# Kernel tuning notes

Measured on AMD Instinct MI355X. Metric: run time of the kernel, lower is better.

The kernel has to match this reference:

```python
import jax, jax.numpy as jnp
import numpy as np

B, L, T = 64, 256, 800
NMEL, PRE, ARNN, DRNN, ENC, ATT, NF, K = 80, 256, 512, 512, 512, 128, 32, 31
ZP = 0.1  # zoneout prob (eval-mode expected-value interpolation)


def setup_inputs() -> dict:
    key = jax.random.key(0)
    ks = iter(jax.random.split(key, 32))
    def p(shape, s=0.05):
        return jax.random.normal(next(ks), shape, dtype=jnp.float32) * s
    inp = {
        'encoder_out': jax.random.normal(next(ks), (B, L, ENC), dtype=jnp.float32),
        'lengths': jax.random.randint(next(ks), (B,), L // 2, L + 1),
        'mels': jax.random.normal(next(ks), (B, T, NMEL), dtype=jnp.float32),
        # prenet: 3 bias-free linears with relu (eval: dropout off)
        'Wp1': p((PRE, NMEL)), 'Wp2': p((PRE, PRE)), 'Wp3': p((PRE, PRE)),
        # attention LSTMCell: input = prenet_dim + enc = 768
        'aWih': p((4 * ARNN, PRE + ENC)), 'aWhh': p((4 * ARNN, ARNN)),
        'abih': jnp.zeros((4 * ARNN,)), 'abhh': jnp.zeros((4 * ARNN,)),
        # decoder LSTMCell: input = att_rnn + enc = 1024
        'dWih': p((4 * DRNN, ARNN + ENC)), 'dWhh': p((4 * DRNN, DRNN)),
        'dbih': jnp.zeros((4 * DRNN,)), 'dbhh': jnp.zeros((4 * DRNN,)),
        # location-sensitive attention (all bias-free)
        'Wq': p((ATT, ARNN)), 'Wm': p((ATT, ENC)),
        'Wconv': p((NF, 2, K)), 'Wloc': p((ATT, NF)), 'v': p((1, ATT)),
        # output projection + gate
        'Wout': p((NMEL, DRNN + ENC)), 'bout': jnp.zeros((NMEL,)),
        'Wgate': p((1, DRNN + ENC)), 'bgate': jnp.zeros((1,)),
    }
    return inp


def _lstm(x, h, c, Wih, Whh, bih, bhh):
    g = x @ Wih.T + h @ Whh.T + (bih + bhh)
    i, f, gg, o = jnp.split(g, 4, axis=-1)
    c2 = jax.nn.sigmoid(f) * c + jax.nn.sigmoid(i) * jnp.tanh(gg)
    return jax.nn.sigmoid(o) * jnp.tanh(c2), c2


def _zoneout(new, old):
    return ZP * old + (1.0 - ZP) * new


def decoder_forward(encoder_out, lengths, mels, Wp1, Wp2, Wp3,
                    aWih, aWhh, abih, abhh, dWih, dWhh, dbih, dbhh,
                    Wq, Wm, Wconv, Wloc, v, Wout, bout, Wgate, bgate):
    b, l, _ = encoder_out.shape
    t = mels.shape[1]
    processed_memory = encoder_out @ Wm.T                       # (B,L,ATT)
    mask = jnp.arange(l)[None, :] >= lengths[:, None]           # True = padded
    # teacher forcing inputs: shift mels right by one zero frame
    dec_in = jnp.concatenate(
        [jnp.zeros((b, 1, NMEL), encoder_out.dtype), mels[:, :t - 1]], axis=1)
    xs = jnp.swapaxes(dec_in, 0, 1)                             # (T,B,NMEL)

    def step(carry, frame):
        ah, ac, dh, dc, ctx, aw, aws = carry
        x = jax.nn.relu(jax.nn.relu(jax.nn.relu(frame @ Wp1.T) @ Wp2.T) @ Wp3.T)
        ah2, ac2 = _lstm(jnp.concatenate([x, ctx], -1), ah, ac, aWih, aWhh, abih, abhh)
        ah2, ac2 = _zoneout(ah2, ah), _zoneout(ac2, ac)
        # location features: conv over (B,2,L)
        aw_cat = jnp.stack([aw, aws], axis=1)
        loc = jax.lax.conv_general_dilated(
            aw_cat, Wconv, window_strides=(1,), padding=[((K - 1) // 2,) * 2],
            dimension_numbers=('NCH', 'OIH', 'NCH'))                # (B,NF,L)
        ploc = jnp.swapaxes(loc, 1, 2) @ Wloc.T                      # (B,L,ATT)
        e = jnp.tanh(ah2[:, None, :] @ Wq.T + processed_memory + ploc)
        energies = jnp.squeeze(e @ v.T, -1)                          # (B,L)
        energies = jnp.where(mask, jnp.float32(-1e9), energies)
        w = jax.nn.softmax(energies, axis=-1)
        ctx2 = jnp.einsum('bl,ble->be', w, encoder_out)
        aws2 = aws + w
        dh2, dc2 = _lstm(jnp.concatenate([ah2, ctx2], -1), dh, dc, dWih, dWhh, dbih, dbhh)
        dh2, dc2 = _zoneout(dh2, dh), _zoneout(dc2, dc)
        dhc = jnp.concatenate([dh2, ctx2], axis=-1)
        mel = dhc @ Wout.T + bout
        gate = jnp.squeeze(dhc @ Wgate.T + bgate, -1)
        return (ah2, ac2, dh2, dc2, ctx2, w, aws2), (mel, gate, w)

    z = lambda *s: jnp.zeros(s, encoder_out.dtype)
    carry0 = (z(b, ARNN), z(b, ARNN), z(b, DRNN), z(b, DRNN), z(b, ENC), z(b, l), z(b, l))
    _, (mel_t, gate_t, align_t) = jax.lax.scan(step, carry0, xs)
    return (jnp.swapaxes(mel_t, 0, 1),      # (B,T,NMEL)
            jnp.swapaxes(gate_t, 0, 1),     # (B,T)
            jnp.swapaxes(align_t, 0, 1))    # (B,T,L)


def reference(encoder_out, lengths, mels, Wp1, Wp2, Wp3,
              aWih, aWhh, abih, abhh, dWih, dWhh, dbih, dbhh,
              Wq, Wm, Wconv, Wloc, v, Wout, bout, Wgate, bgate):
    return decoder_forward(encoder_out, lengths, mels, Wp1, Wp2, Wp3,
                           aWih, aWhh, abih, abhh, dWih, dWhh, dbih, dbhh,
                           Wq, Wm, Wconv, Wloc, v, Wout, bout, Wgate, bgate)
```

## Files before the change

kernel.cpp:

```cpp
#include <hip/hip_runtime.h>


#define DEV_INLINE __device__ __forceinline__

constexpr int TB = 800;

constexpr size_t PMT_O = 0;
constexpr size_t GDT_O = 2097152;
constexpr size_t ENG_O = 2228224;
constexpr size_t WQT_O = 2244608;
constexpr size_t AH_O  = 2310144;
constexpr size_t AC_O  = 2375680;
constexpr size_t DH_O  = 2441216;
constexpr size_t DC_O  = 2506752;
constexpr size_t CTX_O = 2572288;
constexpr size_t AW_O  = 2637824;
constexpr size_t AWS_O = 2670592;
constexpr size_t XB_O  = 2703360;

constexpr size_t MEL_O  = 0;
constexpr size_t GATE_O = 4096000;
constexpr size_t ALG_O  = 4147200;

DEV_INLINE float sigf(float x)     { return 1.0f / (1.0f + __expf(-x)); }
DEV_INLINE float tanhfast(float x) { float e = __expf(2.0f * x); return 1.0f - 2.0f / (e + 1.0f); }

template<int NO>
DEV_INLINE void gseg(float* __restrict__ acc,
                     const float* __restrict__ inT,
                     const float* __restrict__ W, const int ldw, const int wcol0,
                     const int* __restrict__ rows, const int segk0, const int seglen,
                     const int ks, const int ke, const int lane)
{
  const int a0 = ks > segk0 ? ks : segk0;
  const int a1 = (ke < segk0 + seglen) ? ke : (segk0 + seglen);
  if (a0 >= a1) return;
  const float* __restrict__ ip = inT + (size_t)(a0 - segk0) * 64 + lane;
  const int n = a1 - a0;
  const float* wp[NO];
#pragma unroll
  for (int j = 0; j < NO; ++j)
    wp[j] = W + (size_t)rows[j] * ldw + (wcol0 + (a0 - segk0));
  for (int k = 0; k < n; k += 4) {
    const float x0 = ip[(k + 0) * 64];
    const float x1 = ip[(k + 1) * 64];
    const float x2 = ip[(k + 2) * 64];
    const float x3 = ip[(k + 3) * 64];
#pragma unroll
    for (int j = 0; j < NO; ++j)
      acc[j] += x0 * wp[j][k] + x1 * wp[j][k + 1] + x2 * wp[j][k + 2] + x3 * wp[j][k + 3];
  }
}

__global__ __launch_bounds__(256) void init_kernel(const float* __restrict__ Wq,
                                                   float* __restrict__ ws)
{
  const int i = blockIdx.x * 256 + threadIdx.x;
  {
    const int k = i >> 7, a = i & 127;
    ws[WQT_O + i] = Wq[a * 512 + k];
  }
  for (size_t idx = i; idx < 393216; idx += 65536)
    ws[AH_O + idx] = 0.0f;
}

__global__ __launch_bounds__(256) void prenet_kernel(const float* __restrict__ mels,
                                                     const float* __restrict__ Wp1,
                                                     const float* __restrict__ Wp2,
                                                     const float* __restrict__ Wp3,
                                                     float* __restrict__ xb, int t0)
{
  __shared__ float smem[16384];
  const int t = t0 + blockIdx.x;
  const int tid = threadIdx.x;
  const int lane = tid & 63;
  const int wv = __builtin_amdgcn_readfirstlane(tid >> 6);

  if (t == 0) {
    for (int i = tid; i < 5200; i += 256) smem[i] = 0.0f;
  } else {
    for (int i = tid; i < 5120; i += 256) {
      const int b = i / 80, k = i - b * 80;
      smem[k * 65 + b] = mels[((size_t)b * TB + (t - 1)) * 80 + k];
    }
  }
  __syncthreads();

  float va[8][8];
#pragma unroll
  for (int g = 0; g < 8; ++g) {
    const int u0 = wv * 64 + g * 8;
    float acc[8] = {};
    for (int k = 0; k < 80; ++k) {
      const float x = smem[k * 65 + lane];
#pragma unroll
      for (int j = 0; j < 8; ++j) acc[j] += x * Wp1[(u0 + j) * 80 + k];
    }
#pragma unroll
    for (int j = 0; j < 8; ++j) va[g][j] = fmaxf(acc[j], 0.0f);
  }
  __syncthreads();
#pragma unroll
  for (int g = 0; g < 8; ++g)
#pragma unroll
    for (int j = 0; j < 8; ++j) smem[(wv * 64 + g * 8 + j) * 64 + lane] = va[g][j];
  __syncthreads();

#pragma unroll
  for (int g = 0; g < 8; ++g) {
    const int u0 = wv * 64 + g * 8;
    float acc[8] = {};
    for (int k = 0; k < 256; ++k) {
      const float x = smem[k * 64 + lane];
#pragma unroll
      for (int j = 0; j < 8; ++j) acc[j] += x * Wp2[(u0 + j) * 256 + k];
    }
#pragma unroll
    for (int j = 0; j < 8; ++j) va[g][j] = fmaxf(acc[j], 0.0f);
  }
  __syncthreads();
#pragma unroll
  for (int g = 0; g < 8; ++g)
#pragma unroll
    for (int j = 0; j < 8; ++j) smem[(wv * 64 + g * 8 + j) * 64 + lane] = va[g][j];
  __syncthreads();

#pragma unroll
  for (int g = 0; g < 8; ++g) {
    const int u0 = wv * 64 + g * 8;
    float acc[8] = {};
    for (int k = 0; k < 256; ++k) {
      const float x = smem[k * 64 + lane];
#pragma unroll
      for (int j = 0; j < 8; ++j) acc[j] += x * Wp3[(u0 + j) * 256 + k];
    }
#pragma unroll
    for (int j = 0; j < 8; ++j)
      xb[((size_t)blockIdx.x * 256 + (u0 + j)) * 64 + lane] = fmaxf(acc[j], 0.0f);
  }
}

__global__ __launch_bounds__(256) void pm_kernel(const float* __restrict__ enc,
                                                 const float* __restrict__ Wm,
                                                 float* __restrict__ pmT)
{
  __shared__ float encL[64 * 129];
  const int b = blockIdx.x >> 2;
  const int l0 = (blockIdx.x & 3) * 64;
  const int tid = threadIdx.x;
  const int lane = tid & 63;
  const int wv = __builtin_amdgcn_readfirstlane(tid >> 6);

  float acc[4][8];
#pragma unroll
  for (int ai = 0; ai < 4; ++ai)
#pragma unroll
    for (int j = 0; j < 8; ++j) acc[ai][j] = 0.0f;

  for (int kc = 0; kc < 4; ++kc) {
    __syncthreads();
    for (int i = tid; i < 64 * 128; i += 256) {
      const int l = i >> 7, k = i & 127;
      encL[l * 129 + k] = enc[((size_t)b * 256 + l0 + l) * 512 + kc * 128 + k];
    }
    __syncthreads();
#pragma unroll
    for (int ai = 0; ai < 4; ++ai) {
      const int agrp = (ai * 4 + wv) * 8;
      for (int k = 0; k < 128; ++k) {
        const float x = encL[lane * 129 + k];
#pragma unroll
        for (int j = 0; j < 8; ++j)
          acc[ai][j] += x * Wm[(size_t)(agrp + j) * 512 + kc * 128 + k];
      }
    }
  }
#pragma unroll
  for (int ai = 0; ai < 4; ++ai) {
    const int agrp = (ai * 4 + wv) * 8;
#pragma unroll
    for (int j = 0; j < 8; ++j)
      pmT[((size_t)b * 128 + agrp + j) * 256 + l0 + lane] = acc[ai][j];
  }
}

__global__ __launch_bounds__(256) void k_alstm(
    const float* __restrict__ xt,  const float* __restrict__ ctx_i,
    const float* __restrict__ ah_i, const float* __restrict__ ac_i,
    float* __restrict__ ah_o, float* __restrict__ ac_o,
    const float* __restrict__ dh_i,
    const float* __restrict__ aWih, const float* __restrict__ aWhh,
    const float* __restrict__ abih, const float* __restrict__ abhh,
    const float* __restrict__ Wout, const float* __restrict__ bout,
    const float* __restrict__ Wgate, const float* __restrict__ bgate,
    float* __restrict__ out, int t, int do_a, int do_m)
{
  __shared__ float sm[2048];
  const int tid = threadIdx.x;
  const int blk = blockIdx.x;
  const int lane = tid & 63;
  const int wv = __builtin_amdgcn_readfirstlane(tid >> 6);

  if (blk < 256) {
    if (!do_a) return;
    const int u0 = blk * 2;
    int rows[8];
#pragma unroll
    for (int j = 0; j < 8; ++j) rows[j] = u0 + (j >> 2) + 512 * (j & 3);
    float acc[8] = {};
    const int ks = wv * 320, ke = ks + 320;
    gseg<8>(acc, xt,    aWih, 768, 0,   rows, 0,   256, ks, ke, lane);
    gseg<8>(acc, ctx_i, aWih, 768, 256, rows, 256, 512, ks, ke, lane);
    gseg<8>(acc, ah_i,  aWhh, 512, 0,   rows, 768, 512, ks, ke, lane);
#pragma unroll
    for (int j = 0; j < 8; ++j) sm[(wv * 8 + j) * 64 + lane] = acc[j];
    __syncthreads();
    if (tid < 128) {
      const int m = tid & 63, uq = tid >> 6;
      const int u = u0 + uq;
      float g[4];
#pragma unroll
      for (int q = 0; q < 4; ++q) {
        const int j = uq * 4 + q;
        const int row = u + 512 * q;
        g[q] = sm[j * 64 + m] + sm[(8 + j) * 64 + m] + sm[(16 + j) * 64 + m] + sm[(24 + j) * 64 + m]
             + abih[row] + abhh[row];
      }
      const float co = ac_i[u * 64 + m], ho = ah_i[u * 64 + m];
      const float c2 = sigf(g[1]) * co + sigf(g[0]) * tanhfast(g[2]);
      const float h2 = sigf(g[3]) * tanhfast(c2);
      ah_o[u * 64 + m] = 0.1f * ho + 0.9f * h2;
      ac_o[u * 64 + m] = 0.1f * co + 0.9f * c2;
    }
  } else if (do_m && blk < 277) {
    if (blk < 276) {
      const int c0 = (blk - 256) * 4;
      int rows[4] = {c0, c0 + 1, c0 + 2, c0 + 3};
      float acc[4] = {};
      const int ks = wv * 256, ke = ks + 256;
      gseg<4>(acc, dh_i,  Wout, 1024, 0,   rows, 0,   512, ks, ke, lane);
      gseg<4>(acc, ctx_i, Wout, 1024, 512, rows, 512, 512, ks, ke, lane);
#pragma unroll
      for (int j = 0; j < 4; ++j) sm[(wv * 4 + j) * 64 + lane] = acc[j];
      __syncthreads();
      {
        const int m = tid & 63, c = tid >> 6;
        const float val = sm[c * 64 + m] + sm[(4 + c) * 64 + m] + sm[(8 + c) * 64 + m] + sm[(12 + c) * 64 + m]
                        + bout[c0 + c];
        out[MEL_O + ((size_t)m * TB + (t - 1)) * 80 + c0 + c] = val;
      }
    } else {
      float acc[1] = {};
      int rows1[1] = {0};
      const int ks = wv * 256, ke = ks + 256;
      gseg<1>(acc, dh_i,  Wgate, 1024, 0,   rows1, 0,   512, ks, ke, lane);
      gseg<1>(acc, ctx_i, Wgate, 1024, 512, rows1, 512, 512, ks, ke, lane);
      sm[wv * 64 + lane] = acc[0];
      __syncthreads();
      if (tid < 64) {
        const float val = sm[tid] + sm[64 + tid] + sm[128 + tid] + sm[192 + tid] + bgate[0];
        out[GATE_O + (size_t)tid * TB + (t - 1)] = val;
      }
    }
  }
}

__global__ __launch_bounds__(256) void k_energy(
    const float* __restrict__ ah2,  const float* __restrict__ dh_i,
    const float* __restrict__ aw_i, const float* __restrict__ aws_i,
    const float* __restrict__ pmT,  const float* __restrict__ wqT,
    float* __restrict__ gdT, float* __restrict__ eng,
    const float* __restrict__ dWih, const float* __restrict__ dWhh,
    const float* __restrict__ dbih, const float* __restrict__ dbhh,
    const float* __restrict__ Wconv, const float* __restrict__ Wloc,
    const float* __restrict__ v, const int* __restrict__ len)
{
  __shared__ float sm[3584];
  const int tid = threadIdx.x;
  const int blk = blockIdx.x;
  const int lane = tid & 63;
  const int wv = __builtin_amdgcn_readfirstlane(tid >> 6);

  if (blk < 256) {
    const int u0 = blk * 2;
    int rows[8];
#pragma unroll
    for (int j = 0; j < 8; ++j) rows[j] = u0 + (j >> 2) + 512 * (j & 3);
    float acc[8] = {};
    const int ks = wv * 256, ke = ks + 256;
    gseg<8>(acc, ah2,  dWih, 1024, 0, rows, 0,   512, ks, ke, lane);
    gseg<8>(acc, dh_i, dWhh, 512,  0, rows, 512, 512, ks, ke, lane);
#pragma unroll
    for (int j = 0; j < 8; ++j) sm[(wv * 8 + j) * 64 + lane] = acc[j];
    __syncthreads();
    if (tid < 128) {
      const int m = tid & 63, uq = tid >> 6;
      const int u = u0 + uq;
#pragma unroll
      for (int q = 0; q < 4; ++q) {
        const int j = uq * 4 + q;
        const int row = u + 512 * q;
        gdT[(size_t)row * 64 + m] =
            sm[j * 64 + m] + sm[(8 + j) * 64 + m] + sm[(16 + j) * 64 + m] + sm[(24 + j) * 64 + m]
          + dbih[row] + dbhh[row];
      }
    }
  } else {
    const int eb = blk - 256;
    const int b = eb >> 2;
    const int l0 = (eb & 3) * 64;
    float* qL   = sm;
    float* a2L  = sm + 128;
    float* awL  = sm + 640;
    float* awsL = sm + 928;
    float* locL = sm + 1216;
    float* pr   = sm + 3328;

    for (int k = tid; k < 512; k += 256) a2L[k] = ah2[(size_t)k * 64 + b];
    if (tid < 15) { awL[tid] = 0.0f; awsL[tid] = 0.0f; awL[271 + tid] = 0.0f; awsL[271 + tid] = 0.0f; }
    awL[15 + tid]  = aw_i[b * 256 + tid];
    awsL[15 + tid] = aws_i[b * 256 + tid];
    __syncthreads();
    {
      const int a = tid & 127, h = tid >> 7;
      float qp = 0.0f;
      const float* wq = wqT + (size_t)(h * 256) * 128 + a;
      const float* xv = a2L + h * 256;
      for (int k = 0; k < 256; k += 4)
        qp += wq[(k + 0) * 128] * xv[k + 0] + wq[(k + 1) * 128] * xv[k + 1]
            + wq[(k + 2) * 128] * xv[k + 2] + wq[(k + 3) * 128] * xv[k + 3];
      locL[h * 128 + a] = qp;
    }
    __syncthreads();
    if (tid < 128) qL[tid] = locL[tid] + locL[128 + tid];
    __syncthreads();
    {
      float awv[31], awsv[31];
#pragma unroll
      for (int k = 0; k < 31; ++k) { awv[k] = awL[l0 + lane + k]; awsv[k] = awsL[l0 + lane + k]; }
      const int f0 = wv * 8;
      for (int f = f0; f < f0 + 8; ++f) {
        const float* wc = Wconv + f * 62;
        float lf = 0.0f;
#pragma unroll
        for (int k = 0; k < 31; ++k) lf += awv[k] * wc[k] + awsv[k] * wc[31 + k];
        locL[lane * 33 + f] = lf;
      }
    }
    __syncthreads();
    {
      float locv[32];
#pragma unroll
      for (int f = 0; f < 32; ++f) locv[f] = locL[lane * 33 + f];
      float part = 0.0f;
      const int a0 = wv * 32;
      const float* pmp = pmT + (size_t)b * 128 * 256 + l0 + lane;
      for (int a = a0; a < a0 + 32; ++a) {
        float s = qL[a] + pmp[(size_t)a * 256];
        const float* wl = Wloc + a * 32;
#pragma unroll
        for (int f = 0; f < 32; ++f) s += locv[f] * wl[f];
        part += v[a] * tanhfast(s);
      }
      pr[wv * 64 + lane] = part;
    }
    __syncthreads();
    if (tid < 64) {
      float e = pr[tid] + pr[64 + tid] + pr[128 + tid] + pr[192 + tid];
      const int l = l0 + tid;
      if (l >= len[b]) e = -1e9f;
      eng[b * 256 + l] = e;
    }
  }
}

__global__ __launch_bounds__(256) void k_ctx(
    const float* __restrict__ eng, const float* __restrict__ enc,
    const float* __restrict__ aws_i,
    float* __restrict__ ctx_o, float* __restrict__ aw_o, float* __restrict__ aws_o,
    float* __restrict__ out, int t)
{
  __shared__ float sm[896];
  const int tid = threadIdx.x;
  const int lane = tid & 63;
  const int wv = __builtin_amdgcn_readfirstlane(tid >> 6);
  const int b = blockIdx.x >> 2;
  const int ec = blockIdx.x & 3;
  const int e0 = ec * 128;
  float* eL = sm;
  float* wL = sm + 256;
  float* red = sm + 512;
  float* partL = sm + 640;

  eL[tid] = eng[b * 256 + tid];
  __syncthreads();
  float vv = eL[tid];
  for (int mm = 32; mm >= 1; mm >>= 1) vv = fmaxf(vv, __shfl_xor(vv, mm, 64));
  if (lane == 0) red[wv] = vv;
  __syncthreads();
  const float mx = fmaxf(fmaxf(red[0], red[1]), fmaxf(red[2], red[3]));
  const float pex = __expf(eL[tid] - mx);
  wL[tid] = pex;
  float ss = pex;
  for (int mm = 32; mm >= 1; mm >>= 1) ss += __shfl_xor(ss, mm, 64);
  if (lane == 0) red[4 + wv] = ss;
  __syncthreads();
  const float inv = 1.0f / (red[4] + red[5] + red[6] + red[7]);
  {
    const int e_i = tid & 127, lh = tid >> 7;
    float cp = 0.0f;
    const float* ep = enc + ((size_t)b * 256 + lh * 128) * 512 + e0 + e_i;
    for (int l = 0; l < 128; ++l) cp += wL[lh * 128 + l] * ep[(size_t)l * 512];
    partL[lh * 128 + e_i] = cp;
  }
  __syncthreads();
  if (tid < 128) ctx_o[(size_t)(e0 + tid) * 64 + b] = (partL[tid] + partL[128 + tid]) * inv;
  if (ec == 0) {
    const float w = wL[tid] * inv;
    aw_o[b * 256 + tid] = w;
    aws_o[b * 256 + tid] = aws_i[b * 256 + tid] + w;
    out[ALG_O + ((size_t)b * TB + t) * 256 + tid] = w;
  }
}

__global__ __launch_bounds__(256) void k_dfin(
    const float* __restrict__ ctx_o, const float* __restrict__ gdT,
    const float* __restrict__ dh_i,  const float* __restrict__ dc_i,
    float* __restrict__ dh_o, float* __restrict__ dc_o,
    const float* __restrict__ dWih)
{
  __shared__ float sm[2048];
  const int tid = threadIdx.x;
  const int lane = tid & 63;
  const int wv = __builtin_amdgcn_readfirstlane(tid >> 6);
  const int u0 = blockIdx.x * 2;
  int rows[8];
#pragma unroll
  for (int j = 0; j < 8; ++j) rows[j] = u0 + (j >> 2) + 512 * (j & 3);
  float acc[8] = {};
  const int ks = wv * 128, ke = ks + 128;
  gseg<8>(acc, ctx_o, dWih, 1024, 512, rows, 0, 512, ks, ke, lane);
#pragma unroll
  for (int j = 0; j < 8; ++j) sm[(wv * 8 + j) * 64 + lane] = acc[j];
  __syncthreads();
  if (tid < 128) {
    const int m = tid & 63, uq = tid >> 6;
    const int u = u0 + uq;
    float g[4];
#pragma unroll
    for (int q = 0; q < 4; ++q) {
      const int j = uq * 4 + q;
      const int row = u + 512 * q;
      g[q] = sm[j * 64 + m] + sm[(8 + j) * 64 + m] + sm[(16 + j) * 64 + m] + sm[(24 + j) * 64 + m]
           + gdT[(size_t)row * 64 + m];
    }
    const float co = dc_i[u * 64 + m], ho = dh_i[u * 64 + m];
    const float c2 = sigf(g[1]) * co + sigf(g[0]) * tanhfast(g[2]);
    const float h2 = sigf(g[3]) * tanhfast(c2);
    dh_o[u * 64 + m] = 0.1f * ho + 0.9f * h2;
    dc_o[u * 64 + m] = 0.1f * co + 0.9f * c2;
  }
}

extern "C" void kernel_launch(void* const* d_in, const int* in_sizes, int n_in,
                              void* d_out, int out_size, void* d_ws, size_t ws_size,
                              hipStream_t stream)
{
  (void)in_sizes; (void)n_in; (void)out_size;
  const float* enc   = (const float*)d_in[0];
  const int*   len   = (const int*)  d_in[1];
  const float* mels  = (const float*)d_in[2];
  const float* Wp1   = (const float*)d_in[3];
  const float* Wp2   = (const float*)d_in[4];
  const float* Wp3   = (const float*)d_in[5];
  const float* aWih  = (const float*)d_in[6];
  const float* aWhh  = (const float*)d_in[7];
  const float* abih  = (const float*)d_in[8];
  const float* abhh  = (const float*)d_in[9];
  const float* dWih  = (const float*)d_in[10];
  const float* dWhh  = (const float*)d_in[11];
  const float* dbih  = (const float*)d_in[12];
  const float* dbhh  = (const float*)d_in[13];
  const float* Wq    = (const float*)d_in[14];
  const float* Wm    = (const float*)d_in[15];
  const float* Wconv = (const float*)d_in[16];
  const float* Wloc  = (const float*)d_in[17];
  const float* vv    = (const float*)d_in[18];
  const float* Wout  = (const float*)d_in[19];
  const float* bout  = (const float*)d_in[20];
  const float* Wgate = (const float*)d_in[21];
  const float* bgate = (const float*)d_in[22];

  float* ws  = (float*)d_ws;
  float* out = (float*)d_out;

  const size_t need_big = (XB_O + (size_t)TB * 16384) * 4;
  const int CH = (ws_size >= need_big) ? TB : 64;

  init_kernel<<<256, 256, 0, stream>>>(Wq, ws);
  pm_kernel<<<256, 256, 0, stream>>>(enc, Wm, ws + PMT_O);

  for (int t = 0; t <= TB; ++t) {
    if (t < TB && (t % CH) == 0) {
      const int nt = (TB - t) < CH ? (TB - t) : CH;
      prenet_kernel<<<nt, 256, 0, stream>>>(mels, Wp1, Wp2, Wp3, ws + XB_O, t);
    }
    const int cur = t & 1;
    const float* xt = ws + XB_O + (size_t)(t % CH) * 16384;
    float* ah_i = ws + AH_O  + (size_t)cur * 32768;  float* ah_o = ws + AH_O  + (size_t)(cur ^ 1) * 32768;
    float* ac_i = ws + AC_O  + (size_t)cur * 32768;  float* ac_o = ws + AC_O  + (size_t)(cur ^ 1) * 32768;
    float* dh_i = ws + DH_O  + (size_t)cur * 32768;  float* dh_o = ws + DH_O  + (size_t)(cur ^ 1) * 32768;
    float* dc_i = ws + DC_O  + (size_t)cur * 32768;  float* dc_o = ws + DC_O  + (size_t)(cur ^ 1) * 32768;
    float* ctx_i = ws + CTX_O + (size_t)cur * 32768; float* ctx_o = ws + CTX_O + (size_t)(cur ^ 1) * 32768;
    float* aw_i = ws + AW_O  + (size_t)cur * 16384;  float* aw_o = ws + AW_O  + (size_t)(cur ^ 1) * 16384;
    float* aws_i = ws + AWS_O + (size_t)cur * 16384; float* aws_o = ws + AWS_O + (size_t)(cur ^ 1) * 16384;

    k_alstm<<<277, 256, 0, stream>>>(xt, ctx_i, ah_i, ac_i, ah_o, ac_o, dh_i,
                                     aWih, aWhh, abih, abhh,
                                     Wout, bout, Wgate, bgate,
                                     out, t, (t < TB) ? 1 : 0, (t > 0) ? 1 : 0);
    if (t == TB) break;
    k_energy<<<512, 256, 0, stream>>>(ah_o, dh_i, aw_i, aws_i,
                                      ws + PMT_O, ws + WQT_O, ws + GDT_O, ws + ENG_O,
                                      dWih, dWhh, dbih, dbhh, Wconv, Wloc, vv, len);
    k_ctx<<<256, 256, 0, stream>>>(ws + ENG_O, enc, aws_i, ctx_o, aw_o, aws_o, out, t);
    k_dfin<<<256, 256, 0, stream>>>(ctx_o, ws + GDT_O, dh_i, dc_i, dh_o, dc_o, dWih);
  }
}
```

Measured before the change: 87.46 ms.

## Restructure per-step schedule into three fused phase kernels with skewed LSTM steps

Cuts each decode step from four kernel launches to three. The decoder-LSTM finish for step t is fused with the attention-LSTM of step t+1 in one kernel, and the mel/gate projection moves into the energy kernel. Grids are widened so each block handles one hidden unit instead of two, and the context kernel splits the encoder dimension into eight chunks instead of four. These changes aim to reduce launch and serialization overhead and raise parallelism per launch. The cost is more complex buffer indexing and an extra final kernel to emit the last mel and gate frame.

```diff
diff --git a/kernel.cpp b/kernel.cpp
--- a/kernel.cpp
+++ b/kernel.cpp
@@ -184,96 +184,90 @@
   }
 }
 
-__global__ __launch_bounds__(256) void k_alstm(
-    const float* __restrict__ xt,  const float* __restrict__ ctx_i,
-    const float* __restrict__ ah_i, const float* __restrict__ ac_i,
-    float* __restrict__ ah_o, float* __restrict__ ac_o,
-    const float* __restrict__ dh_i,
+__global__ __launch_bounds__(256) void k_phaseA(
+    const float* __restrict__ ctx_t, const float* __restrict__ gdT,
+    const float* __restrict__ dh_p,  const float* __restrict__ dc_p,
+    float* __restrict__ dh_t, float* __restrict__ dc_t,
+    const float* __restrict__ xt, const float* __restrict__ ah_t,
+    const float* __restrict__ ac_t,
+    float* __restrict__ ah_n, float* __restrict__ ac_n,
+    const float* __restrict__ dWih,
     const float* __restrict__ aWih, const float* __restrict__ aWhh,
     const float* __restrict__ abih, const float* __restrict__ abhh,
-    const float* __restrict__ Wout, const float* __restrict__ bout,
-    const float* __restrict__ Wgate, const float* __restrict__ bgate,
-    float* __restrict__ out, int t, int do_a, int do_m)
-{
-  __shared__ float sm[2048];
+    int do_dfin, int do_a)
+{
+  __shared__ float sm[1024];
   const int tid = threadIdx.x;
   const int blk = blockIdx.x;
   const int lane = tid & 63;
   const int wv = __builtin_amdgcn_readfirstlane(tid >> 6);
 
-  if (blk < 256) {
+  if (blk < 512) {
     if (!do_a) return;
-    const int u0 = blk * 2;
-    int rows[8];
-#pragma unroll
-    for (int j = 0; j < 8; ++j) rows[j] = u0 + (j >> 2) + 512 * (j & 3);
-    float acc[8] = {};
+    const int u = blk;
+    int rows[4] = {u, u + 512, u + 1024, u + 1536};
+    float acc[4] = {};
     const int ks = wv * 320, ke = ks + 320;
-    gseg<8>(acc, xt,    aWih, 768, 0,   rows, 0,   256, ks, ke, lane);
-    gseg<8>(acc, ctx_i, aWih, 768, 256, rows, 256, 512, ks, ke, lane);
-    gseg<8>(acc, ah_i,  aWhh, 512, 0,   rows, 768, 512, ks, ke, lane);
-#pragma unroll
-    for (int j = 0; j < 8; ++j) sm[(wv * 8 + j) * 64 + lane] = acc[j];
-    __syncthreads();
-    if (tid < 128) {
-      const int m = tid & 63, uq = tid >> 6;
-      const int u = u0 + uq;
+    gseg<4>(acc, xt,    aWih, 768, 0,   rows, 0,   256, ks, ke, lane);
+    gseg<4>(acc, ctx_t, aWih, 768, 256, rows, 256, 512, ks, ke, lane);
+    gseg<4>(acc, ah_t,  aWhh, 512, 0,   rows, 768, 512, ks, ke, lane);
+#pragma unroll
+    for (int j = 0; j < 4; ++j) sm[(wv * 4 + j) * 64 + lane] = acc[j];
+    __syncthreads();
+    if (tid < 64) {
+      const int m = tid;
       float g[4];
 #pragma unroll
       for (int q = 0; q < 4; ++q) {
-        const int j = uq * 4 + q;
-        const int row = u + 512 * q;
-        g[q] = sm[j * 64 + m] + sm[(8 + j) * 64 + m] + sm[(16 + j) * 64 + m] + sm[(24 + j) * 64 + m]
-             + abih[row] + abhh[row];
-      }
-      const float co = ac_i[u * 64 + m], ho = ah_i[u * 64 + m];
+        g[q] = sm[q * 64 + m] + sm[(4 + q) * 64 + m] + sm[(8 + q) * 64 + m] + sm[(12 + q) * 64 + m]
+             + abih[u + 512 * q] + abhh[u + 512 * q];
+      }
+      const float co = ac_t[u * 64 + m], ho = ah_t[u * 64 + m];
       const float c2 = sigf(g[1]) * co + sigf(g[0]) * tanhfast(g[2]);
       const float h2 = sigf(g[3]) * tanhfast(c2);
-      ah_o[u * 64 + m] = 0.1f * ho + 0.9f * h2;
-      ac_o[u * 64 + m] = 0.1f * co + 0.9f * c2;
-    }
-  } else if (do_m && blk < 277) {
-    if (blk < 276) {
-      const int c0 = (blk - 256) * 4;
-      int rows[4] = {c0, c0 + 1, c0 + 2, c0 + 3};
-      float acc[4] = {};
-      const int ks = wv * 256, ke = ks + 256;
-      gseg<4>(acc, dh_i,  Wout, 1024, 0,   rows, 0,   512, ks, ke, lane);
-      gseg<4>(acc, ctx_i, Wout, 1024, 512, rows, 512, 512, ks, ke, lane);
-#pragma unroll
-      for (int j = 0; j < 4; ++j) sm[(wv * 4 + j) * 64 + lane] = acc[j];
-      __syncthreads();
-      {
-        const int m = tid & 63, c = tid >> 6;
-        const float val = sm[c * 64 + m] + sm[(4 + c) * 64 + m] + sm[(8 + c) * 64 + m] + sm[(12 + c) * 64 + m]
-                        + bout[c0 + c];
-        out[MEL_O + ((size_t)m * TB + (t - 1)) * 80 + c0 + c] = val;
-      }
-    } else {
-      float acc[1] = {};
-      int rows1[1] = {0};
-      const int ks = wv * 256, ke = ks + 256;
-      gseg<1>(acc, dh_i,  Wgate, 1024, 0,   rows1, 0,   512, ks, ke, lane);
-      gseg<1>(acc, ctx_i, Wgate, 1024, 512, rows1, 512, 512, ks, ke, lane);
-      sm[wv * 64 + lane] = acc[0];
-      __syncthreads();
-      if (tid < 64) {
-        const float val = sm[tid] + sm[64 + tid] + sm[128 + tid] + sm[192 + tid] + bgate[0];
-        out[GATE_O + (size_t)tid * TB + (t - 1)] = val;
-      }
-    }
-  }
-}
-
-__global__ __launch_bounds__(256) void k_energy(
-    const float* __restrict__ ah2,  const float* __restrict__ dh_i,
-    const float* __restrict__ aw_i, const float* __restrict__ aws_i,
+      ah_n[u * 64 + m] = 0.1f * ho + 0.9f * h2;
+      ac_n[u * 64 + m] = 0.1f * co + 0.9f * c2;
+    }
+  } else {
+    if (!do_dfin) return;
+    const int u = blk - 512;
+    int rows[4] = {u, u + 512, u + 1024, u + 1536};
+    float acc[4] = {};
+    const int ks = wv * 128, ke = ks + 128;
+    gseg<4>(acc, ctx_t, dWih, 1024, 512, rows, 0, 512, ks, ke, lane);
+#pragma unroll
+    for (int j = 0; j < 4; ++j) sm[(wv * 4 + j) * 64 + lane] = acc[j];
+    __syncthreads();
+    if (tid < 64) {
+      const int m = tid;
+      float g[4];
+#pragma unroll
+      for (int q = 0; q < 4; ++q) {
+        g[q] = sm[q * 64 + m] + sm[(4 + q) * 64 + m] + sm[(8 + q) * 64 + m] + sm[(12 + q) * 64 + m]
+             + gdT[(size_t)(u + 512 * q) * 64 + m];
+      }
+      const float co = dc_p[u * 64 + m], ho = dh_p[u * 64 + m];
+      const float c2 = sigf(g[1]) * co + sigf(g[0]) * tanhfast(g[2]);
+      const float h2 = sigf(g[3]) * tanhfast(c2);
+      dh_t[u * 64 + m] = 0.1f * ho + 0.9f * h2;
+      dc_t[u * 64 + m] = 0.1f * co + 0.9f * c2;
+    }
+  }
+}
+
+__global__ __launch_bounds__(256) void k_phaseB(
+    const float* __restrict__ ah_t, const float* __restrict__ dh_p,
+    const float* __restrict__ ctx_p,
+    const float* __restrict__ aw_p, const float* __restrict__ aws_p,
     const float* __restrict__ pmT,  const float* __restrict__ wqT,
     float* __restrict__ gdT, float* __restrict__ eng,
     const float* __restrict__ dWih, const float* __restrict__ dWhh,
     const float* __restrict__ dbih, const float* __restrict__ dbhh,
     const float* __restrict__ Wconv, const float* __restrict__ Wloc,
-    const float* __restrict__ v, const int* __restrict__ len)
+    const float* __restrict__ v, const int* __restrict__ len,
+    const float* __restrict__ Wout, const float* __restrict__ bout,
+    const float* __restrict__ Wgate, const float* __restrict__ bgate,
+    float* __restrict__ out, int t, int do_m)
 {
   __shared__ float sm[3584];
   const int tid = threadIdx.x;
@@ -281,32 +275,27 @@
   const int lane = tid & 63;
   const int wv = __builtin_amdgcn_readfirstlane(tid >> 6);
 
-  if (blk < 256) {
-    const int u0 = blk * 2;
-    int rows[8];
-#pragma unroll
-    for (int j = 0; j < 8; ++j) rows[j] = u0 + (j >> 2) + 512 * (j & 3);
-    float acc[8] = {};
+  if (blk < 512) {
+    const int u = blk;
+    int rows[4] = {u, u + 512, u + 1024, u + 1536};
+    float acc[4] = {};
     const int ks = wv * 256, ke = ks + 256;
-    gseg<8>(acc, ah2,  dWih, 1024, 0, rows, 0,   512, ks, ke, lane);
-    gseg<8>(acc, dh_i, dWhh, 512,  0, rows, 512, 512, ks, ke, lane);
-#pragma unroll
-    for (int j = 0; j < 8; ++j) sm[(wv * 8 + j) * 64 + lane] = acc[j];
-    __syncthreads();
-    if (tid < 128) {
-      const int m = tid & 63, uq = tid >> 6;
-      const int u = u0 + uq;
+    gseg<4>(acc, ah_t, dWih, 1024, 0, rows, 0,   512, ks, ke, lane);
+    gseg<4>(acc, dh_p, dWhh, 512,  0, rows, 512, 512, ks, ke, lane);
+#pragma unroll
+    for (int j = 0; j < 4; ++j) sm[(wv * 4 + j) * 64 + lane] = acc[j];
+    __syncthreads();
+    if (tid < 64) {
+      const int m = tid;
 #pragma unroll
       for (int q = 0; q < 4; ++q) {
-        const int j = uq * 4 + q;
-        const int row = u + 512 * q;
-        gdT[(size_t)row * 64 + m] =
-            sm[j * 64 + m] + sm[(8 + j) * 64 + m] + sm[(16 + j) * 64 + m] + sm[(24 + j) * 64 + m]
-          + dbih[row] + dbhh[row];
-      }
-    }
-  } else {
-    const int eb = blk - 256;
+        gdT[(size_t)(u + 512 * q) * 64 + m] =
+            sm[q * 64 + m] + sm[(4 + q) * 64 + m] + sm[(8 + q) * 64 + m] + sm[(12 + q) * 64 + m]
+          + dbih[u + 512 * q] + dbhh[u + 512 * q];
+      }
+    }
+  } else if (blk < 768) {
+    const int eb = blk - 512;
     const int b = eb >> 2;
     const int l0 = (eb & 3) * 64;
     float* qL   = sm;
@@ -316,10 +305,10 @@
     float* locL = sm + 1216;
     float* pr   = sm + 3328;
 
-    for (int k = tid; k < 512; k += 256) a2L[k] = ah2[(size_t)k * 64 + b];
+    for (int k = tid; k < 512; k += 256) a2L[k] = ah_t[(size_t)k * 64 + b];
     if (tid < 15) { awL[tid] = 0.0f; awsL[tid] = 0.0f; awL[271 + tid] = 0.0f; awsL[271 + tid] = 0.0f; }
-    awL[15 + tid]  = aw_i[b * 256 + tid];
-    awsL[15 + tid] = aws_i[b * 256 + tid];
+    awL[15 + tid]  = aw_p[b * 256 + tid];
+    awsL[15 + tid] = aws_p[b * 256 + tid];
     __syncthreads();
     {
       const int a = tid & 127, h = tid >> 7;
@@ -371,22 +360,52 @@
       if (l >= len[b]) e = -1e9f;
       eng[b * 256 + l] = e;
     }
-  }
-}
-
-__global__ __launch_bounds__(256) void k_ctx(
+  } else if (do_m && blk < 789) {
+    if (blk < 788) {
+      const int c0 = (blk - 768) * 4;
+      int rows[4] = {c0, c0 + 1, c0 + 2, c0 + 3};
+      float acc[4] = {};
+      const int ks = wv * 256, ke = ks + 256;
+      gseg<4>(acc, dh_p,  Wout, 1024, 0,   rows, 0,   512, ks, ke, lane);
+      gseg<4>(acc, ctx_p, Wout, 1024, 512, rows, 512, 512, ks, ke, lane);
+#pragma unroll
+      for (int j = 0; j < 4; ++j) sm[(wv * 4 + j) * 64 + lane] = acc[j];
+      __syncthreads();
+      {
+        const int m = tid & 63, c = tid >> 6;
+        const float val = sm[c * 64 + m] + sm[(4 + c) * 64 + m] + sm[(8 + c) * 64 + m] + sm[(12 + c) * 64 + m]
+                        + bout[c0 + c];
+        out[MEL_O + ((size_t)m * TB + (t - 1)) * 80 + c0 + c] = val;
+      }
+    } else {
+      float acc[1] = {};
+      int rows1[1] = {0};
+      const int ks = wv * 256, ke = ks + 256;
+      gseg<1>(acc, dh_p,  Wgate, 1024, 0,   rows1, 0,   512, ks, ke, lane);
+      gseg<1>(acc, ctx_p, Wgate, 1024, 512, rows1, 512, 512, ks, ke, lane);
+      sm[wv * 64 + lane] = acc[0];
+      __syncthreads();
+      if (tid < 64) {
+        const float val = sm[tid] + sm[64 + tid] + sm[128 + tid] + sm[192 + tid] + bgate[0];
+        out[GATE_O + (size_t)tid * TB + (t - 1)] = val;
+      }
+    }
+  }
+}
+
+__global__ __launch_bounds__(256) void k_phaseC(
     const float* __restrict__ eng, const float* __restrict__ enc,
-    const float* __restrict__ aws_i,
-    float* __restrict__ ctx_o, float* __restrict__ aw_o, float* __restrict__ aws_o,
+    const float* __restrict__ aws_p,
+    float* __restrict__ ctx_t, float* __restrict__ aw_t, float* __restrict__ aws_t,
     float* __restrict__ out, int t)
 {
   __shared__ float sm[896];
   const int tid = threadIdx.x;
   const int lane = tid & 63;
   const int wv = __builtin_amdgcn_readfirstlane(tid >> 6);
-  const int b = blockIdx.x >> 2;
-  const int ec = blockIdx.x & 3;
-  const int e0 = ec * 128;
+  const int b = blockIdx.x >> 3;
+  const int ec = blockIdx.x & 7;
+  const int e0 = ec * 64;
   float* eL = sm;
   float* wL = sm + 256;
   float* red = sm + 512;
@@ -407,58 +426,63 @@
   __syncthreads();
   const float inv = 1.0f / (red[4] + red[5] + red[6] + red[7]);
   {
-    const int e_i = tid & 127, lh = tid >> 7;
     float cp = 0.0f;
-    const float* ep = enc + ((size_t)b * 256 + lh * 128) * 512 + e0 + e_i;
-    for (int l = 0; l < 128; ++l) cp += wL[lh * 128 + l] * ep[(size_t)l * 512];
-    partL[lh * 128 + e_i] = cp;
-  }
-  __syncthreads();
-  if (tid < 128) ctx_o[(size_t)(e0 + tid) * 64 + b] = (partL[tid] + partL[128 + tid]) * inv;
+    const float* ep = enc + ((size_t)b * 256 + wv * 64) * 512 + e0 + lane;
+    const float* wp = wL + wv * 64;
+    for (int l = 0; l < 64; ++l) cp += wp[l] * ep[(size_t)l * 512];
+    partL[wv * 64 + lane] = cp;
+  }
+  __syncthreads();
+  if (tid < 64)
+    ctx_t[(size_t)(e0 + tid) * 64 + b] =
+        (partL[tid] + partL[64 + tid] + partL[128 + tid] + partL[192 + tid]) * inv;
   if (ec == 0) {
     const float w = wL[tid] * inv;
-    aw_o[b * 256 + tid] = w;
-    aws_o[b * 256 + tid] = aws_i[b * 256 + tid] + w;
+    aw_t[b * 256 + tid] = w;
+    aws_t[b * 256 + tid] = aws_p[b * 256 + tid] + w;
     out[ALG_O + ((size_t)b * TB + t) * 256 + tid] = w;
   }
 }
 
-__global__ __launch_bounds__(256) void k_dfin(
-    const float* __restrict__ ctx_o, const float* __restrict__ gdT,
-    const float* __restrict__ dh_i,  const float* __restrict__ dc_i,
-    float* __restrict__ dh_o, float* __restrict__ dc_o,
-    const float* __restrict__ dWih)
-{
-  __shared__ float sm[2048];
+__global__ __launch_bounds__(256) void k_out_final(
+    const float* __restrict__ dh, const float* __restrict__ ctx,
+    const float* __restrict__ Wout, const float* __restrict__ bout,
+    const float* __restrict__ Wgate, const float* __restrict__ bgate,
+    float* __restrict__ out)
+{
+  __shared__ float sm[1024];
   const int tid = threadIdx.x;
+  const int blk = blockIdx.x;
   const int lane = tid & 63;
   const int wv = __builtin_amdgcn_readfirstlane(tid >> 6);
-  const int u0 = blockIdx.x * 2;
-  int rows[8];
-#pragma unroll
-  for (int j = 0; j < 8; ++j) rows[j] = u0 + (j >> 2) + 512 * (j & 3);
-  float acc[8] = {};
-  const int ks = wv * 128, ke = ks + 128;
-  gseg<8>(acc, ctx_o, dWih, 1024, 512, rows, 0, 512, ks, ke, lane);
-#pragma unroll
-  for (int j = 0; j < 8; ++j) sm[(wv * 8 + j) * 64 + lane] = acc[j];
-  __syncthreads();
-  if (tid < 128) {
-    const int m = tid & 63, uq = tid >> 6;
-    const int u = u0 + uq;
-    float g[4];
-#pragma unroll
-    for (int q = 0; q < 4; ++q) {
-      const int j = uq * 4 + q;
-      const int row = u + 512 * q;
-      g[q] = sm[j * 64 + m] + sm[(8 + j) * 64 + m] + sm[(16 + j) * 64 + m] + sm[(24 + j) * 64 + m]
-           + gdT[(size_t)row * 64 + m];
-    }
-    const float co = dc_i[u * 64 + m], ho = dh_i[u * 64 + m];
-    const float c2 = sigf(g[1]) * co + sigf(g[0]) * tanhfast(g[2]);
-    const float h2 = sigf(g[3]) * tanhfast(c2);
-    dh_o[u * 64 + m] = 0.1f * ho + 0.9f * h2;
-    dc_o[u * 64 + m] = 0.1f * co + 0.9f * c2;
+  if (blk < 20) {
+    const int c0 = blk * 4;
+    int rows[4] = {c0, c0 + 1, c0 + 2, c0 + 3};
+    float acc[4] = {};
+    const int ks = wv * 256, ke = ks + 256;
+    gseg<4>(acc, dh,  Wout, 1024, 0,   rows, 0,   512, ks, ke, lane);
+    gseg<4>(acc, ctx, Wout, 1024, 512, rows, 512, 512, ks, ke, lane);
+#pragma unroll
+    for (int j = 0; j < 4; ++j) sm[(wv * 4 + j) * 64 + lane] = acc[j];
+    __syncthreads();
+    {
+      const int m = tid & 63, c = tid >> 6;
+      const float val = sm[c * 64 + m] + sm[(4 + c) * 64 + m] + sm[(8 + c) * 64 + m] + sm[(12 + c) * 64 + m]
+                      + bout[c0 + c];
+      out[MEL_O + ((size_t)m * TB + (TB - 1)) * 80 + c0 + c] = val;
+    }
+  } else {
+    float acc[1] = {};
+    int rows1[1] = {0};
+    const int ks = wv * 256, ke = ks + 256;
+    gseg<1>(acc, dh,  Wgate, 1024, 0,   rows1, 0,   512, ks, ke, lane);
+    gseg<1>(acc, ctx, Wgate, 1024, 512, rows1, 512, 512, ks, ke, lane);
+    sm[wv * 64 + lane] = acc[0];
+    __syncthreads();
+    if (tid < 64) {
+      const float val = sm[tid] + sm[64 + tid] + sm[128 + tid] + sm[192 + tid] + bgate[0];
+      out[GATE_O + (size_t)tid * TB + (TB - 1)] = val;
+    }
   }
 }
 
@@ -497,33 +521,47 @@
   const size_t need_big = (XB_O + (size_t)TB * 16384) * 4;
   const int CH = (ws_size >= need_big) ? TB : 64;
 
+  float* AH[2]  = {ws + AH_O,  ws + AH_O  + 32768};
+  float* AC[2]  = {ws + AC_O,  ws + AC_O  + 32768};
+  float* DH[2]  = {ws + DH_O,  ws + DH_O  + 32768};
+  float* DC[2]  = {ws + DC_O,  ws + DC_O  + 32768};
+  float* CTX[2] = {ws + CTX_O, ws + CTX_O + 32768};
+  float* AW[2]  = {ws + AW_O,  ws + AW_O  + 16384};
+  float* AWS[2] = {ws + AWS_O, ws + AWS_O + 16384};
+  float* gdT = ws + GDT_O;
+  float* eng = ws + ENG_O;
+
   init_kernel<<<256, 256, 0, stream>>>(Wq, ws);
   pm_kernel<<<256, 256, 0, stream>>>(enc, Wm, ws + PMT_O);
-
-  for (int t = 0; t <= TB; ++t) {
-    if (t < TB && (t % CH) == 0) {
-      const int nt = (TB - t) < CH ? (TB - t) : CH;
-      prenet_kernel<<<nt, 256, 0, stream>>>(mels, Wp1, Wp2, Wp3, ws + XB_O, t);
-    }
-    const int cur = t & 1;
-    const float* xt = ws + XB_O + (size_t)(t % CH) * 16384;
-    float* ah_i = ws + AH_O  + (size_t)cur * 32768;  float* ah_o = ws + AH_O  + (size_t)(cur ^ 1) * 32768;
-    float* ac_i = ws + AC_O  + (size_t)cur * 32768;  float* ac_o = ws + AC_O  + (size_t)(cur ^ 1) * 32768;
-    float* dh_i = ws + DH_O  + (size_t)cur * 32768;  float* dh_o = ws + DH_O  + (size_t)(cur ^ 1) * 32768;
-    float* dc_i = ws + DC_O  + (size_t)cur * 32768;  float* dc_o = ws + DC_O  + (size_t)(cur ^ 1) * 32768;
-    float* ctx_i = ws + CTX_O + (size_t)cur * 32768; float* ctx_o = ws + CTX_O + (size_t)(cur ^ 1) * 32768;
-    float* aw_i = ws + AW_O  + (size_t)cur * 16384;  float* aw_o = ws + AW_O  + (size_t)(cur ^ 1) * 16384;
-    float* aws_i = ws + AWS_O + (size_t)cur * 16384; float* aws_o = ws + AWS_O + (size_t)(cur ^ 1) * 16384;
-
-    k_alstm<<<277, 256, 0, stream>>>(xt, ctx_i, ah_i, ac_i, ah_o, ac_o, dh_i,
-                                     aWih, aWhh, abih, abhh,
-                                     Wout, bout, Wgate, bgate,
-                                     out, t, (t < TB) ? 1 : 0, (t > 0) ? 1 : 0);
-    if (t == TB) break;
-    k_energy<<<512, 256, 0, stream>>>(ah_o, dh_i, aw_i, aws_i,
-                                      ws + PMT_O, ws + WQT_O, ws + GDT_O, ws + ENG_O,
-                                      dWih, dWhh, dbih, dbhh, Wconv, Wloc, vv, len);
-    k_ctx<<<256, 256, 0, stream>>>(ws + ENG_O, enc, aws_i, ctx_o, aw_o, aws_o, out, t);
-    k_dfin<<<256, 256, 0, stream>>>(ctx_o, ws + GDT_O, dh_i, dc_i, dh_o, dc_o, dWih);
-  }
-}
+  {
+    const int nt = (TB < CH) ? TB : CH;
+    prenet_kernel<<<nt, 256, 0, stream>>>(mels, Wp1, Wp2, Wp3, ws + XB_O, 0);
+  }
+
+  k_phaseA<<<1024, 256, 0, stream>>>(CTX[1], gdT, DH[1], DC[1], DH[0], DC[0],
+                                     ws + XB_O, AH[1], AC[1], AH[0], AC[0],
+                                     dWih, aWih, aWhh, abih, abhh, 0, 1);
+
+  for (int t = 0; t < TB; ++t) {
+    const int cur = t & 1, prev = cur ^ 1;
+    const float* xnext = ws + XB_O + (size_t)((t + 1) % CH) * 16384;
+
+    k_phaseB<<<789, 256, 0, stream>>>(AH[cur], DH[prev], CTX[prev],
+                                      AW[prev], AWS[prev],
+                                      ws + PMT_O, ws + WQT_O, gdT, eng,
+                                      dWih, dWhh, dbih, dbhh, Wconv, Wloc, vv, len,
+                                      Wout, bout, Wgate, bgate,
+                                      out, t, (t > 0) ? 1 : 0);
+    k_phaseC<<<512, 256, 0, stream>>>(eng, enc, AWS[prev],
+                                      CTX[cur], AW[cur], AWS[cur], out, t);
+    if (t + 1 < TB && ((t + 1) % CH) == 0) {
+      const int nt = (TB - (t + 1)) < CH ? (TB - (t + 1)) : CH;
+      prenet_kernel<<<nt, 256, 0, stream>>>(mels, Wp1, Wp2, Wp3, ws + XB_O, t + 1);
+    }
+    k_phaseA<<<1024, 256, 0, stream>>>(CTX[cur], gdT, DH[prev], DC[prev], DH[cur], DC[cur],
+                                       xnext, AH[cur], AC[cur], AH[prev], AC[prev],
+                                       dWih, aWih, aWhh, abih, abhh,
+                                       1, (t + 1 < TB) ? 1 : 0);
+  }
+  k_out_final<<<21, 256, 0, stream>>>(DH[1], CTX[1], Wout, bout, Wgate, bgate, out);
+}
```

After: 88.52 ms. About the same (+1.2%).
